# Kernel optimization log

Hardware: AMD Instinct MI355X
Metric: run time of the kernel (lower is better)

Reference implementation:

```python
import jax, jax.numpy as jnp
import numpy as np

NUM_GRAPHS = 4096  # dim_size = batch.max()+1; fixed for jit (fill guarantees max id present)
V, D = 1_000_000, 128


def setup_inputs() -> dict:
    key = jax.random.key(0)
    k1, k2, k3, k4 = jax.random.split(key, 4)
    H = jax.random.normal(k1, (V, D), dtype=jnp.float32)
    batch = jnp.sort(jax.random.randint(k2, (V,), 0, NUM_GRAPHS))
    # nn.Linear(output_size, 1): weight [1, d] -> stored as w [d], bias [1]
    w = jax.random.normal(k3, (D,), dtype=jnp.float32) * 0.05
    b = jax.random.normal(k4, (1,), dtype=jnp.float32) * 0.05
    return {"H": H, "batch": batch, "w": w, "b": b}


def reference(H, batch, w, b):
    # attention_logits = exp(W(H))  -> [V]
    logits = jnp.exp(H @ w + b[0])
    # Z: per-graph normalizer via scatter-sum  -> [num_graphs]
    Z = jax.ops.segment_sum(logits, batch, num_segments=NUM_GRAPHS)
    # segment softmax weights  -> [V]
    alphas = logits / Z[batch]
    # weighted scatter-sum pooling  -> [num_graphs, d]
    return jax.ops.segment_sum(alphas[:, None] * H, batch, num_segments=NUM_GRAPHS)
```

## Files before the change

kernel.cpp:

```cpp
#include <hip/hip_runtime.h>

#define D 128
#define NUM_GRAPHS 4096

__global__ __launch_bounds__(256) void attn_agg_accum(
    const float* __restrict__ H, const int* __restrict__ batch,
    const float* __restrict__ w, const float* __restrict__ b,
    float* __restrict__ S ,
    float* __restrict__ Z ,
    int V)
{
    const int lane = threadIdx.x & 63;
    const int waves_per_block = blockDim.x >> 6;
    const int wave_id = blockIdx.x * waves_per_block + (threadIdx.x >> 6);
    const int total_waves = gridDim.x * waves_per_block;
    const int rows_per_wave = (V + total_waves - 1) / total_waves;

    int row0 = wave_id * rows_per_wave;
    int row1 = row0 + rows_per_wave;
    if (row1 > V) row1 = V;
    if (row0 >= row1) return;

    const float2 w2 = ((const float2*)w)[lane];
    const float bias = b[0];

    float2 acc = make_float2(0.f, 0.f);
    float zacc = 0.f;
    int cur_g = batch[row0];

    for (int v = row0; v < row1; ++v) {
        const float2 h2 = ((const float2*)(H + (size_t)v * D))[lane];
        const int g = batch[v];

        if (g != cur_g) {
            atomicAdd(&S[(size_t)cur_g * D + 2 * lane],     acc.x);
            atomicAdd(&S[(size_t)cur_g * D + 2 * lane + 1], acc.y);
            if (lane == 0) atomicAdd(&Z[cur_g], zacc);
            acc = make_float2(0.f, 0.f);
            zacc = 0.f;
            cur_g = g;
        }

        float dot = h2.x * w2.x + h2.y * w2.y;
        #pragma unroll
        for (int off = 32; off > 0; off >>= 1)
            dot += __shfl_xor(dot, off, 64);

        const float logit = __expf(dot + bias);
        acc.x += logit * h2.x;
        acc.y += logit * h2.y;
        zacc  += logit;
    }
    atomicAdd(&S[(size_t)cur_g * D + 2 * lane],     acc.x);
    atomicAdd(&S[(size_t)cur_g * D + 2 * lane + 1], acc.y);
    if (lane == 0) atomicAdd(&Z[cur_g], zacc);
}

__global__ __launch_bounds__(256) void attn_agg_norm(
    float* __restrict__ out, const float* __restrict__ Z, int n)
{
    const int i = blockIdx.x * blockDim.x + threadIdx.x;
    if (i < n) {
        const int g = i >> 7;
        out[i] = out[i] / Z[g];
    }
}

extern "C" void kernel_launch(void* const* d_in, const int* in_sizes, int n_in,
                              void* d_out, int out_size, void* d_ws, size_t ws_size,
                              hipStream_t stream) {
    const float* H     = (const float*)d_in[0];
    const int*   batch = (const int*)  d_in[1];
    const float* w     = (const float*)d_in[2];
    const float* b     = (const float*)d_in[3];
    float* out = (float*)d_out;
    float* Z   = (float*)d_ws;

    const int V = in_sizes[0] / D;

    hipMemsetAsync(out, 0, (size_t)out_size * sizeof(float), stream);
    hipMemsetAsync(Z,   0, NUM_GRAPHS * sizeof(float), stream);

    attn_agg_accum<<<2048, 256, 0, stream>>>(H, batch, w, b, out, Z, V);

    const int n = NUM_GRAPHS * D;
    attn_agg_norm<<<(n + 255) / 256, 256, 0, stream>>>(out, Z, n);
}
```

Measured before the change: 678.3 us.

## Process two rows per wave with float4 loads and software-prefetched 8-row batches

Each wavefront now splits into two 32-lane halves, each handling alternate rows with 16-byte nontemporal loads, so a single load instruction covers two rows. The main loop register-prefetches the next 8 rows and their graph ids while computing the current batch, interleaving four shuffle reductions and exps to hide latency. Segment-boundary checks are batched with a wave-wide fast path that skips flushes when no graph id changes. This trades extra register pressure and occasional redundant atomic flushes (both halves flush when either changes graph), and assumes an even row count for the tail.

```diff
diff --git a/kernel.cpp b/kernel.cpp
--- a/kernel.cpp
+++ b/kernel.cpp
@@ -2,6 +2,25 @@
 
 #define D 128
 #define NUM_GRAPHS 4096
+
+typedef float v4f __attribute__((ext_vector_type(4)));
+
+__device__ __forceinline__ float dot4(v4f h, v4f w) {
+    return h.x * w.x + h.y * w.y + h.z * w.z + h.w * w.w;
+}
+
+__device__ __forceinline__ void flushv(float* __restrict__ S, float* __restrict__ Z,
+                                       int cur_g, int colbase, bool zlane,
+                                       v4f& acc, float& zacc) {
+    float* p = &S[(size_t)cur_g * D + colbase];
+    atomicAdd(p + 0, acc.x);
+    atomicAdd(p + 1, acc.y);
+    atomicAdd(p + 2, acc.z);
+    atomicAdd(p + 3, acc.w);
+    if (zlane) atomicAdd(&Z[cur_g], zacc);
+    acc = (v4f)(0.f);
+    zacc = 0.f;
+}
 
 __global__ __launch_bounds__(256) void attn_agg_accum(
     const float* __restrict__ H, const int* __restrict__ batch,
@@ -10,50 +29,107 @@
     float* __restrict__ Z ,
     int V)
 {
-    const int lane = threadIdx.x & 63;
-    const int waves_per_block = blockDim.x >> 6;
-    const int wave_id = blockIdx.x * waves_per_block + (threadIdx.x >> 6);
-    const int total_waves = gridDim.x * waves_per_block;
-    const int rows_per_wave = (V + total_waves - 1) / total_waves;
+    const int lane    = threadIdx.x & 63;
+    const int half    = lane >> 5;
+    const int colbase = (lane & 31) << 2;
+    const bool zlane  = (lane & 31) == 0;
 
-    int row0 = wave_id * rows_per_wave;
-    int row1 = row0 + rows_per_wave;
+    const int wave_id     = blockIdx.x * (blockDim.x >> 6) + (threadIdx.x >> 6);
+    const int total_waves = gridDim.x * (blockDim.x >> 6);
+    const int rpw = ((V + total_waves * 8 - 1) / (total_waves * 8)) * 8;
+
+    int row0 = wave_id * rpw;
+    if (row0 >= V) return;
+    int row1 = row0 + rpw;
     if (row1 > V) row1 = V;
-    if (row0 >= row1) return;
 
-    const float2 w2 = ((const float2*)w)[lane];
+    const v4f w4     = ((const v4f*)w)[lane & 31];
     const float bias = b[0];
+    const v4f* __restrict__ Hp = (const v4f*)H;
 
-    float2 acc = make_float2(0.f, 0.f);
+    v4f acc   = (v4f)(0.f);
     float zacc = 0.f;
-    int cur_g = batch[row0];
+    int cur_g = batch[row0 + half];
 
-    for (int v = row0; v < row1; ++v) {
-        const float2 h2 = ((const float2*)(H + (size_t)v * D))[lane];
-        const int g = batch[v];
+    int v = row0;
+    v4f h0, h1, h2, h3;
+    int g0, g1, g2, g3;
+    if (v + 8 <= row1) {
+        h0 = __builtin_nontemporal_load(&Hp[(size_t)(v + 0) * 32 + lane]);
+        h1 = __builtin_nontemporal_load(&Hp[(size_t)(v + 2) * 32 + lane]);
+        h2 = __builtin_nontemporal_load(&Hp[(size_t)(v + 4) * 32 + lane]);
+        h3 = __builtin_nontemporal_load(&Hp[(size_t)(v + 6) * 32 + lane]);
+        g0 = batch[v + 0 + half];
+        g1 = batch[v + 2 + half];
+        g2 = batch[v + 4 + half];
+        g3 = batch[v + 6 + half];
+    }
 
-        if (g != cur_g) {
-            atomicAdd(&S[(size_t)cur_g * D + 2 * lane],     acc.x);
-            atomicAdd(&S[(size_t)cur_g * D + 2 * lane + 1], acc.y);
-            if (lane == 0) atomicAdd(&Z[cur_g], zacc);
-            acc = make_float2(0.f, 0.f);
-            zacc = 0.f;
-            cur_g = g;
+    while (v + 8 <= row1) {
+        const int nv = v + 8;
+        v4f n0 = h0, n1 = h1, n2 = h2, n3 = h3;
+        int m0 = g0, m1 = g1, m2 = g2, m3 = g3;
+        if (nv + 8 <= row1) {
+            n0 = __builtin_nontemporal_load(&Hp[(size_t)(nv + 0) * 32 + lane]);
+            n1 = __builtin_nontemporal_load(&Hp[(size_t)(nv + 2) * 32 + lane]);
+            n2 = __builtin_nontemporal_load(&Hp[(size_t)(nv + 4) * 32 + lane]);
+            n3 = __builtin_nontemporal_load(&Hp[(size_t)(nv + 6) * 32 + lane]);
+            m0 = batch[nv + 0 + half];
+            m1 = batch[nv + 2 + half];
+            m2 = batch[nv + 4 + half];
+            m3 = batch[nv + 6 + half];
         }
 
-        float dot = h2.x * w2.x + h2.y * w2.y;
+        float d0 = dot4(h0, w4);
+        float d1 = dot4(h1, w4);
+        float d2 = dot4(h2, w4);
+        float d3 = dot4(h3, w4);
         #pragma unroll
-        for (int off = 32; off > 0; off >>= 1)
-            dot += __shfl_xor(dot, off, 64);
+        for (int off = 16; off > 0; off >>= 1) {
+            d0 += __shfl_xor(d0, off, 64);
+            d1 += __shfl_xor(d1, off, 64);
+            d2 += __shfl_xor(d2, off, 64);
+            d3 += __shfl_xor(d3, off, 64);
+        }
 
-        const float logit = __expf(dot + bias);
-        acc.x += logit * h2.x;
-        acc.y += logit * h2.y;
-        zacc  += logit;
+        const float l0 = __expf(d0 + bias);
+        const float l1 = __expf(d1 + bias);
+        const float l2 = __expf(d2 + bias);
+        const float l3 = __expf(d3 + bias);
+
+        const int diff = (g0 ^ cur_g) | (g1 ^ cur_g) | (g2 ^ cur_g) | (g3 ^ cur_g);
+        if (__builtin_expect(!__any(diff), 1)) {
+            acc += h0 * l0 + h1 * l1 + h2 * l2 + h3 * l3;
+            zacc += l0 + l1 + l2 + l3;
+        } else {
+            if (__any(g0 ^ cur_g)) { flushv(S, Z, cur_g, colbase, zlane, acc, zacc); cur_g = g0; }
+            acc += h0 * l0; zacc += l0;
+            if (__any(g1 ^ cur_g)) { flushv(S, Z, cur_g, colbase, zlane, acc, zacc); cur_g = g1; }
+            acc += h1 * l1; zacc += l1;
+            if (__any(g2 ^ cur_g)) { flushv(S, Z, cur_g, colbase, zlane, acc, zacc); cur_g = g2; }
+            acc += h2 * l2; zacc += l2;
+            if (__any(g3 ^ cur_g)) { flushv(S, Z, cur_g, colbase, zlane, acc, zacc); cur_g = g3; }
+            acc += h3 * l3; zacc += l3;
+        }
+
+        h0 = n0; h1 = n1; h2 = n2; h3 = n3;
+        g0 = m0; g1 = m1; g2 = m2; g3 = m3;
+        v = nv;
     }
-    atomicAdd(&S[(size_t)cur_g * D + 2 * lane],     acc.x);
-    atomicAdd(&S[(size_t)cur_g * D + 2 * lane + 1], acc.y);
-    if (lane == 0) atomicAdd(&Z[cur_g], zacc);
+
+    for (; v + 2 <= row1; v += 2) {
+        v4f h = __builtin_nontemporal_load(&Hp[(size_t)v * 32 + lane]);
+        int g = batch[v + half];
+        float d = dot4(h, w4);
+        #pragma unroll
+        for (int off = 16; off > 0; off >>= 1)
+            d += __shfl_xor(d, off, 64);
+        const float l = __expf(d + bias);
+        if (__any(g ^ cur_g)) { flushv(S, Z, cur_g, colbase, zlane, acc, zacc); cur_g = g; }
+        acc += h * l; zacc += l;
+    }
+
+    flushv(S, Z, cur_g, colbase, zlane, acc, zacc);
 }
 
 __global__ __launch_bounds__(256) void attn_agg_norm(
```

Result: faster. 646.8 us (-4.6%).
